# Performance work log

Hardware: AMD Instinct MI355X
Metric: run time of the kernel (lower is better)

## Reference

```python
import jax, jax.numpy as jnp
import numpy as np

N_NODES = 50000
N_EDGES = 600000
F_IN = 128
H = 128
NUM_GRAPHS = 64
SELF_LOOP_W = 2.0  # improved=True


def setup_inputs() -> dict:
    key = jax.random.key(0)
    ks = jax.random.split(key, 16)
    x = jax.random.normal(ks[0], (N_NODES, F_IN), dtype=jnp.float32)
    edge_index = jax.random.randint(ks[1], (2, N_EDGES), 0, N_NODES, dtype=jnp.int64)
    batch_index = jnp.sort(jax.random.randint(ks[2], (N_NODES,), 0, NUM_GRAPHS, dtype=jnp.int64))
    edge_weight = jax.random.uniform(ks[3], (N_EDGES,), dtype=jnp.float32)
    def lin(k, fin, fout):
        s = 1.0 / np.sqrt(fin)
        kw, kb = jax.random.split(k)
        W = jax.random.uniform(kw, (fin, fout), minval=-s, maxval=s, dtype=jnp.float32)
        b = jax.random.uniform(kb, (fout,), minval=-s, maxval=s, dtype=jnp.float32)
        return W, b
    W0, b0 = lin(ks[4], F_IN, H)
    W1, b1 = lin(ks[5], H, H)
    W2, b2 = lin(ks[6], H, H)
    W3, b3 = lin(ks[7], H, H)
    Wout, bout = lin(ks[8], 2 * H, 1)
    return dict(x=x, edge_index=edge_index, batch_index=batch_index, edge_weight=edge_weight,
                W0=W0, b0=b0, W1=W1, b1=b1, W2=W2, b2=b2, W3=W3, b3=b3, Wout=Wout, bout=bout)


def reference(x, edge_index, batch_index, edge_weight, W0, b0, W1, b1, W2, b2, W3, b3, Wout, bout):
    N = x.shape[0]
    loop = jnp.arange(N)
    src = jnp.concatenate([edge_index[0], loop])  # [E+N]
    dst = jnp.concatenate([edge_index[1], loop])
    w = jnp.concatenate([edge_weight, jnp.full((N,), SELF_LOOP_W, dtype=x.dtype)])
    # symmetric GCN normalization: deg over destination, norm = d^-1/2[src]*w*d^-1/2[dst]
    deg = jax.ops.segment_sum(w, dst, num_segments=N)
    dinv = jnp.where(deg > 0, jax.lax.rsqrt(deg), 0.0)
    norm = dinv[src] * w * dinv[dst]  # [E+N]

    def conv(h, W, b):
        h = h @ W  # dense transform before aggregation
        msg = h[src] * norm[:, None]
        return jax.ops.segment_sum(msg, dst, num_segments=N) + b

    h = jnp.tanh(conv(x, W0, b0))
    h = jnp.tanh(conv(h, W1, b1))
    h = jnp.tanh(conv(h, W2, b2))
    h = jnp.tanh(conv(h, W3, b3))

    gmax = jax.ops.segment_max(h, batch_index, num_segments=NUM_GRAPHS)
    gmax = jnp.where(jnp.isfinite(gmax), gmax, 0.0)  # guard empty graphs
    cnt = jax.ops.segment_sum(jnp.ones((N,), dtype=h.dtype), batch_index, num_segments=NUM_GRAPHS)
    gmean = jax.ops.segment_sum(h, batch_index, num_segments=NUM_GRAPHS) / jnp.maximum(cnt, 1.0)[:, None]
    hidden = jnp.concatenate([gmax, gmean], axis=1)  # [B, 2H]
    out = hidden @ Wout + bout  # [B, 1]
    return out, hidden
```

## Files before the change

### kernel.cpp

```cpp
#include <hip/hip_runtime.h>
#include <hip/hip_bf16.h>
#include <hip/hip_fp16.h>

typedef __hip_bfloat16 bf16;
typedef _Float16 half8 __attribute__((ext_vector_type(8)));
typedef float f32x4 __attribute__((ext_vector_type(4)));

#define FDIM 128
#define SELF_W 2.0f
#define NGRAPH 64
#define DEG_SCALE 1048576.0f
#define DEG_MASK  ((1ull<<44) - 1ull)

__device__ __forceinline__ float b2f(bf16 v){ return __bfloat162float(v); }

__device__ __forceinline__ float rdf(const void* p, long long i, int f32){
  return f32 ? ((const float*)p)[i] : b2f(((const bf16*)p)[i]);
}
__device__ __forceinline__ int rdi(const void* p, long long i, int i64){
  return i64 ? (int)(((const long long*)p)[i]) : ((const int*)p)[i];
}

__device__ __forceinline__ float tanh_fast(float x){
  float ax = fabsf(x);
  float e  = __expf(-2.0f*ax);
  float r  = (1.0f - e) * __builtin_amdgcn_rcpf(1.0f + e);
  return copysignf(r, x);
}

struct PtrPack { const void* p[10]; };
__global__ __launch_bounds__(256) void k_setup(PtrPack pk, float* __restrict__ pf,
                                               _Float16* __restrict__ wt,
                                               unsigned long long* __restrict__ packed,
                                               const void* __restrict__ bat,
                                               unsigned* __restrict__ gstart,
                                               const unsigned short* __restrict__ x16,
                                               const int* __restrict__ ei32,
                                               int* __restrict__ flags_out,
                                               int N){
  __shared__ int cbig, codd, sf32, si64;
  int tid = threadIdx.x;
  if (tid == 0){ cbig = 0; codd = 0; }
  __syncthreads();
  for (int i = tid; i < 4096; i += 256){
    int e = (x16[i] >> 7) & 0xFF;
    if (e >= 134) atomicAdd(&cbig, 1);
  }
  for (int i = tid; i < 512; i += 256){
    if (ei32[2*i + 1] != 0) atomicAdd(&codd, 1);
  }
  __syncthreads();
  if (tid == 0){
    sf32 = (cbig >= 64) ? 1 : 0;
    si64 = (codd < 8)  ? 1 : 0;
    if (blockIdx.x == 0){ flags_out[0] = sf32; flags_out[1] = si64; }
  }
  __syncthreads();
  int f32 = sf32, i64 = si64;

  const int sz[10]  = {16384,16384,16384,16384,128,128,128,128,256,1};
  const int dst[10] = {0,16384,32768,49152,65536,65664,65792,65920,66048,66304};
  int i = blockIdx.x*blockDim.x + tid;
  if (i < 66305){
    int seg = 0, rem = i;
    while (rem >= sz[seg]){ rem -= sz[seg]; seg++; }
    float v = rdf(pk.p[seg], rem, f32);
    pf[dst[seg] + rem] = v;
    if (seg < 4){
      int k = rem >> 7, n = rem & 127;
      wt[seg*16384 + n*128 + k] = (_Float16)v;
    }
  }
  int stride = gridDim.x*blockDim.x;
  for (int j = i; j < N; j += stride)
    packed[j] = (unsigned long long)(SELF_W * DEG_SCALE);
  if (blockIdx.x == gridDim.x - 1){
    __shared__ unsigned s[NGRAPH+1];
    int g = tid;
    if (g <= NGRAPH){
      int lo = 0, hi = N;
      while (lo < hi){ int mid = (lo + hi) >> 1; if (rdi(bat, mid, i64) < g) lo = mid + 1; else hi = mid; }
      s[g] = (unsigned)lo;
    }
    __syncthreads();
    if (g <= NGRAPH) gstart[g] = s[g];
  }
}

__global__ void k_edge_deg(const void* __restrict__ ei, const void* __restrict__ ew,
                           unsigned long long* __restrict__ packed,
                           unsigned* __restrict__ rank,
                           int E, int N, const int* __restrict__ flags){
  int e0 = 2*(blockIdx.x*blockDim.x + threadIdx.x);
  if (e0 >= E) return;
  int i64 = flags[1], f32 = flags[0];
  int e1 = e0 + 1;
  bool h1 = (e1 < E);
  int d0 = rdi(ei, (long long)E + e0, i64);
  int d1 = h1 ? rdi(ei, (long long)E + e1, i64) : 0;
  float w0 = rdf(ew, e0, f32);
  float w1 = h1 ? rdf(ew, e1, f32) : 0.f;
  unsigned r0 = 0u, r1 = 0u;
  if ((unsigned)d0 < (unsigned)N){
    unsigned long long add = (1ull << 44) |
        (unsigned long long)__float2uint_rn(w0 * DEG_SCALE);
    r0 = (unsigned)(atomicAdd(&packed[d0], add) >> 44);
  }
  if (h1 && (unsigned)d1 < (unsigned)N){
    unsigned long long add = (1ull << 44) |
        (unsigned long long)__float2uint_rn(w1 * DEG_SCALE);
    r1 = (unsigned)(atomicAdd(&packed[d1], add) >> 44);
  }
  rank[e0] = r0;
  if (h1) rank[e1] = r1;
}

__device__ __forceinline__ unsigned wave_incl_scan(unsigned v){
  int lane = threadIdx.x & 63;
  #pragma unroll
  for (int d = 1; d < 64; d <<= 1){
    unsigned t = __shfl_up(v, d, 64);
    if (lane >= d) v += t;
  }
  return v;
}

__global__ __launch_bounds__(256) void k_scan_pre(const unsigned long long* __restrict__ packed,
                                                  float* __restrict__ dinv,
                                                  float* __restrict__ swv,
                                                  unsigned* __restrict__ bsum,
                                                  unsigned* __restrict__ epk, unsigned Epad,
                                                  int N){
  __shared__ unsigned wsh[4];
  int tid = threadIdx.x, lane = tid & 63, wid = tid >> 6;
  unsigned gid = blockIdx.x*blockDim.x + tid, gstr = gridDim.x*blockDim.x;
  for (unsigned j = gid; j < Epad; j += gstr) epk[j] = 0u;
  int i0 = blockIdx.x*1024 + tid*4;
  unsigned tsum = 0u;
  #pragma unroll
  for (int j = 0; j < 4; j++){
    int i = i0 + j;
    if (i < N){
      unsigned long long pv = packed[i];
      tsum += ((unsigned)(pv >> 44) + 7u) & ~7u;
      float d = (float)(pv & DEG_MASK) * (1.0f / DEG_SCALE);
      float di = (d > 0.f) ? rsqrtf(d) : 0.f;
      dinv[i] = di;
      swv[i]  = di * di * SELF_W;
    }
  }
  #pragma unroll
  for (int d = 1; d < 64; d <<= 1) tsum += __shfl_down(tsum, d, 64);
  if (lane == 0) wsh[wid] = tsum;
  __syncthreads();
  if (tid == 0) bsum[blockIdx.x] = wsh[0] + wsh[1] + wsh[2] + wsh[3];
}

__global__ __launch_bounds__(256) void k_scan_fin(const unsigned long long* __restrict__ packed,
                                                  const unsigned* __restrict__ bsum,
                                                  unsigned* __restrict__ off, int N, int NB){
  __shared__ unsigned wsh[4];
  __shared__ unsigned sbase, stot;
  int tid = threadIdx.x, lane = tid & 63, wid = tid >> 6;
  if (tid < 64){
    unsigned v = (tid < NB) ? bsum[tid] : 0u;
    unsigned isc = wave_incl_scan(v);
    if (tid == (int)blockIdx.x) sbase = isc - v;
    if (tid == 63) stot = isc;
  }
  __syncthreads();
  int i0 = blockIdx.x*1024 + tid*4;
  unsigned v0=0u,v1=0u,v2=0u,v3=0u;
  if (i0+0 < N) v0 = ((unsigned)(packed[i0+0] >> 44) + 7u) & ~7u;
  if (i0+1 < N) v1 = ((unsigned)(packed[i0+1] >> 44) + 7u) & ~7u;
  if (i0+2 < N) v2 = ((unsigned)(packed[i0+2] >> 44) + 7u) & ~7u;
  if (i0+3 < N) v3 = ((unsigned)(packed[i0+3] >> 44) + 7u) & ~7u;
  unsigned tsum = v0+v1+v2+v3;
  unsigned isc = wave_incl_scan(tsum);
  if (lane == 63) wsh[wid] = isc;
  __syncthreads();
  unsigned wbase = 0u;
  #pragma unroll
  for (int w = 0; w < 4; w++) if (w < wid) wbase += wsh[w];
  unsigned ex = sbase + wbase + (isc - tsum);
  if (i0+0 < N) off[i0+0] = ex;
  if (i0+1 < N) off[i0+1] = ex + v0;
  if (i0+2 < N) off[i0+2] = ex + v0 + v1;
  if (i0+3 < N) off[i0+3] = ex + v0 + v1 + v2;
  if (blockIdx.x == gridDim.x - 1 && tid == 0) off[N] = stot;
}

__global__ void k_bucket(const void* __restrict__ ei, const void* __restrict__ ew,
                         const float* __restrict__ dinv,
                         const unsigned* __restrict__ off,
                         const unsigned* __restrict__ rank,
                         unsigned* __restrict__ epk,
                         int E, unsigned Epad, int N, const int* __restrict__ flags){
  int e0 = 2*(blockIdx.x*blockDim.x + threadIdx.x);
  if (e0 >= E) return;
  int i64 = flags[1], f32 = flags[0];
  #pragma unroll
  for (int j = 0; j < 2; j++){
    int e = e0 + j;
    if (e >= E) break;
    int s_ = rdi(ei, e, i64);
    int d  = rdi(ei, (long long)E + e, i64);
    if ((unsigned)s_ >= (unsigned)N || (unsigned)d >= (unsigned)N) continue;
    unsigned pos = off[d] + rank[e];
    if (pos < Epad){
      float coef = dinv[s_] * rdf(ew, e, f32) * dinv[d];
      _Float16 ch = (_Float16)coef;
      unsigned cu = (unsigned)__builtin_bit_cast(unsigned short, ch);
      epk[pos] = ((unsigned)s_ & 0xffffu) | (cu << 16);
    }
  }
}

template<int MODE>
__global__ __launch_bounds__(256) void k_gemm(const void* __restrict__ in,
                                              const _Float16* __restrict__ WT,
                                              _Float16* __restrict__ outp, int N,
                                              size_t pstride,
                                              const int* __restrict__ flags){
  __shared__ _Float16 sout[4*16*136];
  int tid  = threadIdx.x;
  int wid  = tid >> 6, lane = tid & 63;
  int ln   = lane & 15, quad = lane >> 4;
  int row0 = blockIdx.x * 64;
  int rowA = row0 + wid*16 + ln;
  int rA   = (rowA < N) ? rowA : (N > 0 ? N-1 : 0);

  half8 af[4];
  if (MODE == 1){
    const _Float16* src = (const _Float16*)in;
    #pragma unroll
    for (int kc = 0; kc < 4; kc++)
      af[kc] = *(const half8*)(src + (size_t)kc*pstride + (size_t)rA*32 + quad*8);
  } else {
    if (flags[0]){
      const float* src = (const float*)in + (size_t)rA*FDIM + quad*8;
      #pragma unroll
      for (int kc = 0; kc < 4; kc++){
        float4 a = *(const float4*)(src + kc*32);
        float4 b = *(const float4*)(src + kc*32 + 4);
        half8 h; h[0]=(_Float16)a.x; h[1]=(_Float16)a.y; h[2]=(_Float16)a.z; h[3]=(_Float16)a.w;
        h[4]=(_Float16)b.x; h[5]=(_Float16)b.y; h[6]=(_Float16)b.z; h[7]=(_Float16)b.w;
        af[kc] = h;
      }
    } else {
      const unsigned short* src = (const unsigned short*)in + (size_t)rA*FDIM + quad*8;
      #pragma unroll
      for (int kc = 0; kc < 4; kc++){
        ushort4 u0 = *(const ushort4*)(src + kc*32);
        ushort4 u1 = *(const ushort4*)(src + kc*32 + 4);
        half8 h;
        h[0]=(_Float16)__uint_as_float((unsigned)u0.x<<16);
        h[1]=(_Float16)__uint_as_float((unsigned)u0.y<<16);
        h[2]=(_Float16)__uint_as_float((unsigned)u0.z<<16);
        h[3]=(_Float16)__uint_as_float((unsigned)u0.w<<16);
        h[4]=(_Float16)__uint_as_float((unsigned)u1.x<<16);
        h[5]=(_Float16)__uint_as_float((unsigned)u1.y<<16);
        h[6]=(_Float16)__uint_as_float((unsigned)u1.z<<16);
        h[7]=(_Float16)__uint_as_float((unsigned)u1.w<<16);
        af[kc] = h;
      }
    }
  }

  f32x4 acc[8];
  #pragma unroll
  for (int nt = 0; nt < 8; nt++) acc[nt] = (f32x4){0.f,0.f,0.f,0.f};

  #pragma unroll
  for (int kc = 0; kc < 4; kc++){
    #pragma unroll
    for (int nt = 0; nt < 8; nt++){
      half8 bf = *(const half8*)(WT + (size_t)(nt*16 + ln)*FDIM + kc*32 + quad*8);
      acc[nt] = __builtin_amdgcn_mfma_f32_16x16x32_f16(af[kc], bf, acc[nt], 0, 0, 0);
    }
  }

  _Float16* so = sout + wid*2176;
  #pragma unroll
  for (int nt = 0; nt < 8; nt++)
    #pragma unroll
    for (int reg = 0; reg < 4; reg++)
      so[(quad*4 + reg)*136 + nt*16 + ln] = (_Float16)acc[nt][reg];
  __syncthreads();

  #pragma unroll
  for (int c = 0; c < 4; c++){
    int chunk = tid + c*256;
    int r = chunk >> 4, co = (chunk & 15)*8;
    int row = row0 + r;
    if (row < N){
      half8 v = *(const half8*)(sout + (r>>4)*2176 + (r&15)*136 + co);
      *(half8*)(outp + (size_t)(co>>5)*pstride + (size_t)row*32 + (co & 31)) = v;
    }
  }
}

__global__ __launch_bounds__(256) void k_agg(const _Float16* __restrict__ tp,
                                             const float* __restrict__ swv,
                                             const unsigned* __restrict__ off,
                                             const unsigned* __restrict__ epk,
                                             const float* __restrict__ bias,
                                             _Float16* __restrict__ hp,
                                             int N, size_t pstride){
  int tid  = threadIdx.x;
  int wv   = tid >> 6, lane = tid & 63;
  int quad = lane >> 4, ql = lane & 15;
  int panel = blockIdx.y;
  int n = blockIdx.x*16 + wv*4 + quad;
  bool valid = (n < N);
  int nn = valid ? n : 0;
  const _Float16* tpp = tp + (size_t)panel*pstride;
  const _Float16* myt = tpp + ql*2;

  float sw = swv[nn];
  float2 sv = __half22float2(*(const __half2*)(myt + (size_t)nn*32));
  float a0 = sw * sv.x, a1 = sw * sv.y;
  float b0 = 0.f, b1 = 0.f;

  unsigned beg = off[nn];
  unsigned end = valid ? off[nn+1] : beg;
  if (beg < end){
    uint4 p0 = *(const uint4*)(epk + beg);
    uint4 p1 = *(const uint4*)(epk + beg + 4);
    for (unsigned i = beg; i < end; i += 8){
      unsigned ni  = i + 8;
      unsigned pre = (ni < end) ? ni : beg;
      uint4 q0 = *(const uint4*)(epk + pre);
      uint4 q1 = *(const uint4*)(epk + pre + 4);
      unsigned vs[8] = {p0.x,p0.y,p0.z,p0.w,p1.x,p1.y,p1.z,p1.w};
      __half2 tv[8];
      #pragma unroll
      for (int j = 0; j < 8; j++)
        tv[j] = *(const __half2*)(myt + (size_t)(vs[j] & 0xffffu)*32);
      #pragma unroll
      for (int j = 0; j < 8; j++){
        float w = (float)__builtin_bit_cast(_Float16, (unsigned short)(vs[j] >> 16));
        float2 tf = __half22float2(tv[j]);
        if (j & 1){ b0 += w * tf.x; b1 += w * tf.y; }
        else      { a0 += w * tf.x; a1 += w * tf.y; }
      }
      p0 = q0; p1 = q1;
    }
  }
  a0 += b0; a1 += b1;
  int cc = panel*32 + ql*2;
  a0 = tanh_fast(a0 + bias[cc]);
  a1 = tanh_fast(a1 + bias[cc+1]);
  if (valid)
    *(__half2*)(hp + (size_t)panel*pstride + (size_t)n*32 + ql*2) = __floats2half2_rn(a0, a1);
}

__global__ __launch_bounds__(256) void k_pool_part(const _Float16* __restrict__ hp,
                                                   const unsigned* __restrict__ gstart,
                                                   float* __restrict__ pmax,
                                                   float* __restrict__ psum,
                                                   size_t pstride){
  int g = blockIdx.x >> 4, sub = blockIdx.x & 15;
  int tid = threadIdx.x;
  int col = tid & 127, half_ = tid >> 7;
  const _Float16* hpp = hp + (size_t)(col >> 5)*pstride + (col & 31);
  unsigned s0 = gstart[g], s1 = gstart[g+1];
  float m = -INFINITY, sm = 0.f;
  for (unsigned n = s0 + sub*2 + half_; n < s1; n += 32){
    float v = (float)hpp[(size_t)n*32];
    m = fmaxf(m, v); sm += v;
  }
  __shared__ float shm[256], shs[256];
  shm[tid] = m; shs[tid] = sm;
  __syncthreads();
  if (half_ == 0){
    m  = fmaxf(m, shm[tid + 128]);
    sm += shs[tid + 128];
    int slot = (g*16 + sub)*128 + col;
    pmax[slot] = m;
    psum[slot] = sm;
  }
}

__global__ __launch_bounds__(256) void k_pool_out(const float* __restrict__ pmax,
                                                  const float* __restrict__ psum,
                                                  const unsigned* __restrict__ gstart,
                                                  const float* __restrict__ Wout,
                                                  const float* __restrict__ bout,
                                                  void* __restrict__ outp,
                                                  const int* __restrict__ flags){
  int g = blockIdx.x, tid = threadIdx.x;
  int col = tid & 127, sub = tid >> 7;
  unsigned cnt = gstart[g+1] - gstart[g];
  float val;
  if (sub == 0){
    float m = -INFINITY;
    #pragma unroll
    for (int j = 0; j < 16; j++) m = fmaxf(m, pmax[(g*16 + j)*128 + col]);
    val = (cnt > 0 && m > -INFINITY) ? m : 0.f;
  } else {
    float s = 0.f;
    #pragma unroll
    for (int j = 0; j < 16; j++) s += psum[(g*16 + j)*128 + col];
    val = s / (float)(cnt ? cnt : 1u);
  }
  int hcol = sub*128 + col;
  int f32out = flags[0];
  int hidx = NGRAPH + g*(2*FDIM) + hcol;
  if (f32out) ((float*)outp)[hidx] = val;
  else        ((bf16*)outp)[hidx] = __float2bfloat16(val);

  __shared__ float red[256];
  red[hcol] = val * Wout[hcol];
  __syncthreads();
  for (int s = 128; s > 0; s >>= 1){
    if (tid < s) red[tid] += red[tid + s];
    __syncthreads();
  }
  if (tid == 0){
    float o = red[0] + bout[0];
    if (f32out) ((float*)outp)[g] = o;
    else        ((bf16*)outp)[g] = __float2bfloat16(o);
  }
}

extern "C" void kernel_launch(void* const* d_in, const int* in_sizes, int n_in,
                              void* d_out, int out_size, void* d_ws, size_t ws_size,
                              hipStream_t stream){
  int N = in_sizes[0] / FDIM;
  int E = in_sizes[3];
  int NB = (N + 1023) / 1024;
  unsigned Epad = (unsigned)E + 8u*(unsigned)N;
  size_t pstride = (size_t)N * 32;

  char* p = (char*)d_ws;
  auto alloc = [&](size_t bytes){ char* r = p; p += (bytes + 255) & ~(size_t)255; return r; };
  int*       flags  = (int*)      alloc(16);
  float*     pf     = (float*)    alloc((size_t)(66305 + 64)*4);
  _Float16*  wt     = (_Float16*) alloc((size_t)4*FDIM*FDIM*2);
  unsigned long long* packed = (unsigned long long*)alloc((size_t)N*8);
  float*     dinv   = (float*)    alloc((size_t)N*4);
  float*     swv    = (float*)    alloc((size_t)N*4);
  unsigned*  off    = (unsigned*) alloc((size_t)(N+1)*4);
  unsigned*  bsum   = (unsigned*) alloc((size_t)128*4);
  unsigned*  rank   = (unsigned*) alloc((size_t)E*4);
  unsigned*  epk    = (unsigned*) alloc((size_t)Epad*4);
  _Float16*  th     = (_Float16*) alloc((size_t)N*FDIM*2);
  _Float16*  hh     = (_Float16*) alloc((size_t)N*FDIM*2);
  float*     pmax   = (float*)    alloc((size_t)NGRAPH*16*128*4);
  float*     psum   = (float*)    alloc((size_t)NGRAPH*16*128*4);
  unsigned*  gstart = (unsigned*) alloc((size_t)(NGRAPH+1)*4);

  float* bf_[4] = {pf + 65536, pf + 65664, pf + 65792, pf + 65920};
  float* Woutf  = pf + 66048;
  float* boutf  = pf + 66304;

  PtrPack pk;
  pk.p[0]=d_in[4]; pk.p[1]=d_in[6]; pk.p[2]=d_in[8]; pk.p[3]=d_in[10];
  pk.p[4]=d_in[5]; pk.p[5]=d_in[7]; pk.p[6]=d_in[9]; pk.p[7]=d_in[11];
  pk.p[8]=d_in[12]; pk.p[9]=d_in[13];
  k_setup<<<(66305 + 255)/256, 256, 0, stream>>>(pk, pf, wt, packed, d_in[2], gstart,
                                                 (const unsigned short*)d_in[0],
                                                 (const int*)d_in[1], flags, N);
  int gE2 = (E + 511)/512;
  k_edge_deg<<<gE2, 256, 0, stream>>>(d_in[1], d_in[3], packed, rank, E, N, flags);
  k_scan_pre<<<NB, 256, 0, stream>>>(packed, dinv, swv, bsum, epk, Epad, N);
  k_scan_fin<<<NB, 256, 0, stream>>>(packed, bsum, off, N, NB);
  k_bucket<<<gE2, 256, 0, stream>>>(d_in[1], d_in[3], dinv, off, rank, epk, E, Epad, N, flags);

  int gG = (N + 63)/64;
  int ng4 = (N + 15)/16;
  dim3 gA(ng4, 4);

  k_gemm<0><<<gG, 256, 0, stream>>>(d_in[0], wt + 0*16384, th, N, pstride, flags);
  k_agg<<<gA, 256, 0, stream>>>(th, swv, off, epk, bf_[0], hh, N, pstride);
  for (int l = 1; l < 4; l++){
    k_gemm<1><<<gG, 256, 0, stream>>>(hh, wt + (size_t)l*16384, th, N, pstride, flags);
    k_agg<<<gA, 256, 0, stream>>>(th, swv, off, epk, bf_[l], hh, N, pstride);
  }

  k_pool_part<<<16*NGRAPH, 256, 0, stream>>>(hh, gstart, pmax, psum, pstride);
  k_pool_out<<<NGRAPH, 256, 0, stream>>>(pmax, psum, gstart, Woutf, boutf, d_out, flags);
}
```

Baseline: 371.3 us.

## Switch feature buffers to row-major layout and widen aggregation gathers to half8

Replaces the 4-panel column-split feature layout with a plain row-major [N,128] fp16 layout across gemm, aggregation and pooling. The aggregation kernel now processes all 128 features per node in one pass with 16-byte gathers per lane, so each edge list is read once instead of once per panel. This trades fewer, wider memory requests for higher register use per thread and fewer waves in flight.

```diff
diff --git a/kernel.cpp b/kernel.cpp
--- a/kernel.cpp
+++ b/kernel.cpp
@@ -220,7 +220,6 @@
 __global__ __launch_bounds__(256) void k_gemm(const void* __restrict__ in,
                                               const _Float16* __restrict__ WT,
                                               _Float16* __restrict__ outp, int N,
-                                              size_t pstride,
                                               const int* __restrict__ flags){
   __shared__ _Float16 sout[4*16*136];
   int tid  = threadIdx.x;
@@ -232,10 +231,10 @@
 
   half8 af[4];
   if (MODE == 1){
-    const _Float16* src = (const _Float16*)in;
+    const _Float16* src = (const _Float16*)in + (size_t)rA*FDIM + quad*8;
     #pragma unroll
     for (int kc = 0; kc < 4; kc++)
-      af[kc] = *(const half8*)(src + (size_t)kc*pstride + (size_t)rA*32 + quad*8);
+      af[kc] = *(const half8*)(src + kc*32);
   } else {
     if (flags[0]){
       const float* src = (const float*)in + (size_t)rA*FDIM + quad*8;
@@ -295,7 +294,7 @@
     int row = row0 + r;
     if (row < N){
       half8 v = *(const half8*)(sout + (r>>4)*2176 + (r&15)*136 + co);
-      *(half8*)(outp + (size_t)(co>>5)*pstride + (size_t)row*32 + (co & 31)) = v;
+      *(half8*)(outp + (size_t)row*FDIM + co) = v;
     }
   }
 }
@@ -306,21 +305,22 @@
                                              const unsigned* __restrict__ epk,
                                              const float* __restrict__ bias,
                                              _Float16* __restrict__ hp,
-                                             int N, size_t pstride){
+                                             int N){
   int tid  = threadIdx.x;
   int wv   = tid >> 6, lane = tid & 63;
   int quad = lane >> 4, ql = lane & 15;
-  int panel = blockIdx.y;
   int n = blockIdx.x*16 + wv*4 + quad;
   bool valid = (n < N);
   int nn = valid ? n : 0;
-  const _Float16* tpp = tp + (size_t)panel*pstride;
-  const _Float16* myt = tpp + ql*2;
-
-  float sw = swv[nn];
-  float2 sv = __half22float2(*(const __half2*)(myt + (size_t)nn*32));
-  float a0 = sw * sv.x, a1 = sw * sv.y;
-  float b0 = 0.f, b1 = 0.f;
+  const _Float16* myt = tp + ql*8;
+
+  float acc[8];
+  {
+    float sw = swv[nn];
+    half8 sv = *(const half8*)(myt + (size_t)nn*FDIM);
+    #pragma unroll
+    for (int k = 0; k < 8; k++) acc[k] = sw * (float)sv[k];
+  }
 
   unsigned beg = off[nn];
   unsigned end = valid ? off[nn+1] : beg;
@@ -333,41 +333,44 @@
       uint4 q0 = *(const uint4*)(epk + pre);
       uint4 q1 = *(const uint4*)(epk + pre + 4);
       unsigned vs[8] = {p0.x,p0.y,p0.z,p0.w,p1.x,p1.y,p1.z,p1.w};
-      __half2 tv[8];
+      half8 tv[8];
       #pragma unroll
       for (int j = 0; j < 8; j++)
-        tv[j] = *(const __half2*)(myt + (size_t)(vs[j] & 0xffffu)*32);
+        tv[j] = *(const half8*)(myt + (size_t)(vs[j] & 0xffffu)*FDIM);
       #pragma unroll
       for (int j = 0; j < 8; j++){
         float w = (float)__builtin_bit_cast(_Float16, (unsigned short)(vs[j] >> 16));
-        float2 tf = __half22float2(tv[j]);
-        if (j & 1){ b0 += w * tf.x; b1 += w * tf.y; }
-        else      { a0 += w * tf.x; a1 += w * tf.y; }
+        #pragma unroll
+        for (int k = 0; k < 8; k++)
+          acc[k] += w * (float)tv[j][k];
       }
       p0 = q0; p1 = q1;
     }
   }
-  a0 += b0; a1 += b1;
-  int cc = panel*32 + ql*2;
-  a0 = tanh_fast(a0 + bias[cc]);
-  a1 = tanh_fast(a1 + bias[cc+1]);
+  int cc = ql*8;
+  float4 b0 = *(const float4*)(bias + cc);
+  float4 b1 = *(const float4*)(bias + cc + 4);
+  float bb[8] = {b0.x,b0.y,b0.z,b0.w,b1.x,b1.y,b1.z,b1.w};
+  half8 out;
+  #pragma unroll
+  for (int k = 0; k < 8; k++)
+    out[k] = (_Float16)tanh_fast(acc[k] + bb[k]);
   if (valid)
-    *(__half2*)(hp + (size_t)panel*pstride + (size_t)n*32 + ql*2) = __floats2half2_rn(a0, a1);
+    *(half8*)(hp + (size_t)nn*FDIM + ql*8) = out;
 }
 
 __global__ __launch_bounds__(256) void k_pool_part(const _Float16* __restrict__ hp,
                                                    const unsigned* __restrict__ gstart,
                                                    float* __restrict__ pmax,
-                                                   float* __restrict__ psum,
-                                                   size_t pstride){
+                                                   float* __restrict__ psum){
   int g = blockIdx.x >> 4, sub = blockIdx.x & 15;
   int tid = threadIdx.x;
   int col = tid & 127, half_ = tid >> 7;
-  const _Float16* hpp = hp + (size_t)(col >> 5)*pstride + (col & 31);
+  const _Float16* hpp = hp + col;
   unsigned s0 = gstart[g], s1 = gstart[g+1];
   float m = -INFINITY, sm = 0.f;
   for (unsigned n = s0 + sub*2 + half_; n < s1; n += 32){
-    float v = (float)hpp[(size_t)n*32];
+    float v = (float)hpp[(size_t)n*FDIM];
     m = fmaxf(m, v); sm += v;
   }
   __shared__ float shm[256], shs[256];
@@ -431,7 +434,6 @@
   int E = in_sizes[3];
   int NB = (N + 1023) / 1024;
   unsigned Epad = (unsigned)E + 8u*(unsigned)N;
-  size_t pstride = (size_t)N * 32;
 
   char* p = (char*)d_ws;
   auto alloc = [&](size_t bytes){ char* r = p; p += (bytes + 255) & ~(size_t)255; return r; };
@@ -469,16 +471,15 @@
   k_bucket<<<gE2, 256, 0, stream>>>(d_in[1], d_in[3], dinv, off, rank, epk, E, Epad, N, flags);
 
   int gG = (N + 63)/64;
-  int ng4 = (N + 15)/16;
-  dim3 gA(ng4, 4);
-
-  k_gemm<0><<<gG, 256, 0, stream>>>(d_in[0], wt + 0*16384, th, N, pstride, flags);
-  k_agg<<<gA, 256, 0, stream>>>(th, swv, off, epk, bf_[0], hh, N, pstride);
+  int gA = (N + 15)/16;
+
+  k_gemm<0><<<gG, 256, 0, stream>>>(d_in[0], wt + 0*16384, th, N, flags);
+  k_agg<<<gA, 256, 0, stream>>>(th, swv, off, epk, bf_[0], hh, N);
   for (int l = 1; l < 4; l++){
-    k_gemm<1><<<gG, 256, 0, stream>>>(hh, wt + (size_t)l*16384, th, N, pstride, flags);
-    k_agg<<<gA, 256, 0, stream>>>(th, swv, off, epk, bf_[l], hh, N, pstride);
-  }
-
-  k_pool_part<<<16*NGRAPH, 256, 0, stream>>>(hh, gstart, pmax, psum, pstride);
+    k_gemm<1><<<gG, 256, 0, stream>>>(hh, wt + (size_t)l*16384, th, N, flags);
+    k_agg<<<gA, 256, 0, stream>>>(th, swv, off, epk, bf_[l], hh, N);
+  }
+
+  k_pool_part<<<16*NGRAPH, 256, 0, stream>>>(hh, gstart, pmax, psum);
   k_pool_out<<<NGRAPH, 256, 0, stream>>>(pmax, psum, gstart, Woutf, boutf, d_out, flags);
 }
```

Result: faster. 362.6 us, median of 2 (-2.3%).
